# Kernel tuning notes

Hardware: AMD Instinct MI355X
Metric: run time of the kernel (lower is better)

## Reference

```python
import jax, jax.numpy as jnp
import numpy as np

E, H, I, K, T = 8, 1024, 2816, 2, 2048


def setup_inputs() -> dict:
    key = jax.random.key(0)
    k1, k2, k3, k4, k5, k6 = jax.random.split(key, 6)
    hidden_states = jax.random.normal(k1, (T, H), dtype=jnp.float32)
    top_k_indices = jax.random.randint(k2, (T, K), 0, E, dtype=jnp.int32)
    raw = jax.random.uniform(k3, (T, K), dtype=jnp.float32) + 0.1
    top_k_values = raw / jnp.sum(raw, axis=-1, keepdims=True)  # router softmax-like weights
    scale = 1.0 / np.sqrt(H)
    w_gate = jax.random.normal(k4, (E, H, I), dtype=jnp.float32) * scale
    w_up = jax.random.normal(k5, (E, H, I), dtype=jnp.float32) * scale
    w_down = jax.random.normal(k6, (E, I, H), dtype=jnp.float32) * (1.0 / np.sqrt(I))
    return {
        "hidden_states": hidden_states,
        "top_k_indices": top_k_indices,
        "top_k_values": top_k_values,
        "w_gate": w_gate,
        "w_up": w_up,
        "w_down": w_down,
    }


def reference(hidden_states, top_k_indices, top_k_values, w_gate, w_up, w_down):
    # Each expert: SwiGLU FFN  down( silu(x @ gate) * (x @ up) )
    # Run every expert on every token (dense reference for grouped-GEMM dispatch),
    # then combine with the per-token top-k routing weights.
    def expert(wg, wu, wd):
        g = jnp.matmul(hidden_states, wg)          # [T, I]
        u = jnp.matmul(hidden_states, wu)          # [T, I]
        return jnp.matmul(jax.nn.silu(g) * u, wd)  # [T, H]

    y = jax.vmap(expert)(w_gate, w_up, w_down)     # [E, T, H]

    t = hidden_states.shape[0]
    # comb[t, e] = sum over k of top_k_values[t, k] where top_k_indices[t, k] == e
    comb = jnp.zeros((t, w_gate.shape[0]), dtype=hidden_states.dtype)
    comb = comb.at[jnp.arange(t)[:, None], top_k_indices].add(top_k_values)
    out = jnp.einsum('te,eth->th', comb, y)        # weighted combine -> [T, H]
    return out
```

## Files before the change

kernel.cpp:

```cpp
#include <hip/hip_runtime.h>
#include <stdint.h>

#define T_TOK 2048
#define KTOP  2
#define NEXP  8
#define HDIM  1024
#define IDIM  2816

#define NPAIR 4096

#define BM        128
#define MAX_TILES 40
#define NPP       (NPAIR + BM)
#define BN2       128
#define BK2       32
#define BN3       64
#define BK3       64
#define GUB       (MAX_TILES * (IDIM / BN2))
#define CVB       ((IDIM / 64) * (HDIM / 64) * NEXP)

#define R1BM   256
#define R1T    24
#define R1NPP  (NPAIR + R1BM)
#define R1BN2  128
#define R1BK2  32
#define R1BKp2 40
#define R1BN3  64
#define R1BK3  64
#define R1BKp3 72

typedef __attribute__((ext_vector_type(8))) short short8;
typedef __attribute__((ext_vector_type(4))) float floatx4;

__device__ __forceinline__ unsigned short f2bf(float f) {
  unsigned int u = __float_as_uint(f);
  u += 0x7fffu + ((u >> 16) & 1u);
  return (unsigned short)(u >> 16);
}

__device__ __forceinline__ unsigned int pkbf(float a, float b) {
  unsigned int r;
  asm volatile("v_cvt_pk_bf16_f32 %0, %1, %2" : "=v"(r) : "v"(a), "v"(b));
  return r;
}

__device__ __forceinline__ void glds16(const unsigned short* g, unsigned short* l) {
  __builtin_amdgcn_global_load_lds(
      (const __attribute__((address_space(1))) unsigned int*)g,
      (__attribute__((address_space(3))) unsigned int*)l, 16, 0, 0);
}

__device__ __forceinline__ int xcd_tile(int bx0) {
  return (bx0 & 7) * (MAX_TILES / 8) + (bx0 >> 3);
}

__global__ void setup_kernel(const int* __restrict__ idx,
                             const float* __restrict__ vals,
                             int* __restrict__ hdr,
                             int* __restrict__ stok,
                             float* __restrict__ sw, int bm) {
  __shared__ int cnt[NEXP];
  __shared__ int off[NEXP];
  int tid = threadIdx.x;
  if (tid < NEXP) cnt[tid] = 0;
  __syncthreads();
  for (int p = tid; p < NPAIR; p += blockDim.x) atomicAdd(&cnt[idx[p]], 1);
  __syncthreads();
  if (tid == 0) {
    int s = 0, nt = 0;
    for (int e = 0; e < NEXP; ++e) {
      off[e] = s;
      int n = cnt[e];
      for (int t0 = 0; t0 < n; t0 += bm) {
        hdr[nt] = e;
        hdr[64 + nt] = s + t0;
        hdr[128 + nt] = s + n;
        nt++;
      }
      s += n;
    }
    for (; nt < 64; ++nt) hdr[nt] = -1;
  }
  __syncthreads();
  for (int p = tid; p < NPAIR; p += blockDim.x) {
    int e = idx[p];
    int pos = atomicAdd(&off[e], 1);
    stok[pos] = p / KTOP;
    sw[pos] = vals[p];
  }
}

__global__ void gather_kernel(const float* __restrict__ hidden,
                              const int* __restrict__ stok,
                              unsigned short* __restrict__ Xs) {
  int p = blockIdx.x;
  int t = stok[p];
  const float4* src = reinterpret_cast<const float4*>(hidden + (size_t)t * HDIM);
  float4 v = src[threadIdx.x];
  uint2 q;
  q.x = pkbf(v.x, v.y);
  q.y = pkbf(v.z, v.w);
  *reinterpret_cast<uint2*>(Xs + (size_t)p * HDIM + threadIdx.x * 4) = q;
}

__global__ __launch_bounds__(256) void convert_kernel(
    const float* __restrict__ wg, const float* __restrict__ wu,
    const float* __restrict__ wd, unsigned short* __restrict__ wgT,
    unsigned short* __restrict__ wuT, unsigned short* __restrict__ wdT,
    int zoff) {
  __shared__ float ls[64][65];
  int z = blockIdx.z + zoff;
  int e = blockIdx.y;
  int M = (z == 2) ? IDIM : HDIM;
  int N = (z == 2) ? HDIM : IDIM;
  const float* src = (z == 0 ? wg : z == 1 ? wu : wd) + (size_t)e * M * N;
  unsigned short* dst = (z == 0 ? wgT : z == 1 ? wuT : wdT) + (size_t)e * M * N;
  int ntx = N >> 6;
  int n0 = (blockIdx.x % ntx) << 6;
  int m0 = (blockIdx.x / ntx) << 6;
  int t = threadIdx.x;
  int rr = t >> 4, cc = (t & 15) * 4;
#pragma unroll
  for (int i = 0; i < 4; ++i) {
    int r = rr + i * 16;
    float4 v = *reinterpret_cast<const float4*>(src + (size_t)(m0 + r) * N + n0 + cc);
    ls[r][cc] = v.x; ls[r][cc + 1] = v.y; ls[r][cc + 2] = v.z; ls[r][cc + 3] = v.w;
  }
  __syncthreads();
  int mc = (t & 7) * 8, nn = t >> 3;
#pragma unroll
  for (int i = 0; i < 2; ++i) {
    int n = nn + i * 32;
    uint4 q;
    q.x = pkbf(ls[mc][n],     ls[mc + 1][n]);
    q.y = pkbf(ls[mc + 2][n], ls[mc + 3][n]);
    q.z = pkbf(ls[mc + 4][n], ls[mc + 5][n]);
    q.w = pkbf(ls[mc + 6][n], ls[mc + 7][n]);
    *reinterpret_cast<uint4*>(dst + (size_t)(n0 + n) * M + m0 + mc) = q;
  }
}

__global__ __launch_bounds__(256, 2) void gateup_kernel(
    const unsigned short* __restrict__ Xs, const unsigned short* __restrict__ wgT,
    const unsigned short* __restrict__ wuT, const int* __restrict__ hdr,
    const float* __restrict__ sw_g, unsigned short* __restrict__ Act,
    const float* __restrict__ wd, unsigned short* __restrict__ wdT) {
  __shared__ __align__(16) char smem[25088];

  if (blockIdx.x >= GUB) {
    int cb = blockIdx.x - GUB;
    int e = cb / ((IDIM / 64) * (HDIM / 64));
    int bq = cb % ((IDIM / 64) * (HDIM / 64));
    const int ntx = HDIM >> 6;
    int n0 = (bq % ntx) << 6;
    int m0 = (bq / ntx) << 6;
    const float* src = wd + (size_t)e * IDIM * HDIM;
    unsigned short* dst = wdT + (size_t)e * IDIM * HDIM;
    float (*ls)[65] = reinterpret_cast<float(*)[65]>(smem);
    int t = threadIdx.x;
    int rr = t >> 4, cc = (t & 15) * 4;
#pragma unroll
    for (int i = 0; i < 4; ++i) {
      int r = rr + i * 16;
      float4 v = *reinterpret_cast<const float4*>(src + (size_t)(m0 + r) * HDIM + n0 + cc);
      ls[r][cc] = v.x; ls[r][cc + 1] = v.y; ls[r][cc + 2] = v.z; ls[r][cc + 3] = v.w;
    }
    __syncthreads();
    int mc = (t & 7) * 8, nn = t >> 3;
#pragma unroll
    for (int i = 0; i < 2; ++i) {
      int n = nn + i * 32;
      uint4 q;
      q.x = pkbf(ls[mc][n],     ls[mc + 1][n]);
      q.y = pkbf(ls[mc + 2][n], ls[mc + 3][n]);
      q.z = pkbf(ls[mc + 4][n], ls[mc + 5][n]);
      q.w = pkbf(ls[mc + 6][n], ls[mc + 7][n]);
      *reinterpret_cast<uint4*>(dst + (size_t)(n0 + n) * IDIM + m0 + mc) = q;
    }
    return;
  }

  int mx = blockIdx.x % MAX_TILES;
  int ny = blockIdx.x / MAX_TILES;
  int bx = xcd_tile(mx);
  int e = hdr[bx];
  if (e < 0) return;
  int row0 = hdr[64 + bx];
  int rowlim = hdr[128 + bx] - row0;
  int n0 = ny * BN2;

  unsigned short* As = reinterpret_cast<unsigned short*>(smem);
  unsigned short* Bg = reinterpret_cast<unsigned short*>(smem + 8192);
  unsigned short* Bu = reinterpret_cast<unsigned short*>(smem + 16384);
  float* sw = reinterpret_cast<float*>(smem + 24576);

  int tid = threadIdx.x, lane = tid & 63, wave = tid >> 6;
  if (tid < BM) sw[tid] = sw_g[row0 + tid];

  const unsigned short* wgb = wgT + (size_t)e * IDIM * HDIM;
  const unsigned short* wub = wuT + (size_t)e * IDIM * HDIM;

  floatx4 accg[4][4], accu[4][4];
  floatx4 zz = {0.f, 0.f, 0.f, 0.f};
#pragma unroll
  for (int a = 0; a < 4; ++a)
#pragma unroll
    for (int b = 0; b < 4; ++b) { accg[a][b] = zz; accu[a][b] = zz; }

  int wm = (wave >> 1) * 64, wn = (wave & 1) * 64;
  int lr = lane >> 2;
  int lk = (((lane & 3) ^ ((lr >> 1) & 3)) * 8);
  int fr = lane & 15;
  int fq = (((lane >> 4) ^ ((fr >> 1) & 3)) * 8);

  for (int kb = 0; kb < HDIM; kb += BK2) {
#pragma unroll
    for (int it = 0; it < 2; ++it) {
      int c = wave * 2 + it;
      glds16(Xs  + (size_t)(row0 + c * 16 + lr) * HDIM + kb + lk, &As[c * 512]);
      glds16(wgb + (size_t)(n0  + c * 16 + lr) * HDIM + kb + lk, &Bg[c * 512]);
      glds16(wub + (size_t)(n0  + c * 16 + lr) * HDIM + kb + lk, &Bu[c * 512]);
    }
    __syncthreads();

    short8 af[4], bg8[4], bu8[4];
#pragma unroll
    for (int x = 0; x < 4; ++x) {
      af[x]  = *reinterpret_cast<const short8*>(&As[(wm + x * 16 + fr) * BK2 + fq]);
      bg8[x] = *reinterpret_cast<const short8*>(&Bg[(wn + x * 16 + fr) * BK2 + fq]);
      bu8[x] = *reinterpret_cast<const short8*>(&Bu[(wn + x * 16 + fr) * BK2 + fq]);
    }
#pragma unroll
    for (int tm = 0; tm < 4; ++tm)
#pragma unroll
      for (int tn = 0; tn < 4; ++tn) {
        accg[tm][tn] = __builtin_amdgcn_mfma_f32_16x16x32_bf16(af[tm], bg8[tn], accg[tm][tn], 0, 0, 0);
        accu[tm][tn] = __builtin_amdgcn_mfma_f32_16x16x32_bf16(af[tm], bu8[tn], accu[tm][tn], 0, 0, 0);
      }
    __syncthreads();
  }

#pragma unroll
  for (int tm = 0; tm < 4; ++tm)
#pragma unroll
    for (int tn = 0; tn < 4; ++tn)
#pragma unroll
      for (int r = 0; r < 4; ++r) {
        int rl = wm + tm * 16 + (lane >> 4) * 4 + r;
        if (rl < rowlim) {
          int col = n0 + wn + tn * 16 + fr;
          float g = accg[tm][tn][r];
          float u = accu[tm][tn][r];
          float s = g / (1.f + __expf(-g));
          Act[(size_t)(row0 + rl) * IDIM + col] = f2bf(s * u * sw[rl]);
        }
      }
}

__global__ __launch_bounds__(256, 3) void down_kernel(
    const unsigned short* __restrict__ Act, const unsigned short* __restrict__ wdT,
    const int* __restrict__ hdr, const int* __restrict__ stok,
    float* __restrict__ out) {
  int bx = xcd_tile(blockIdx.x);
  int e = hdr[bx];
  if (e < 0) return;
  int row0 = hdr[64 + bx];
  int rowlim = hdr[128 + bx] - row0;
  int n0 = blockIdx.y * BN3;

  __shared__ __align__(16) unsigned short As[BM * BK3];
  __shared__ __align__(16) unsigned short Bd[BN3 * BK3];
  __shared__ int stk[BM];

  int tid = threadIdx.x, lane = tid & 63, wave = tid >> 6;
  if (tid < BM) stk[tid] = stok[row0 + tid];

  const unsigned short* wdb = wdT + (size_t)e * HDIM * IDIM;

  floatx4 acc[4][2];
  floatx4 zz = {0.f, 0.f, 0.f, 0.f};
#pragma unroll
  for (int a = 0; a < 4; ++a) { acc[a][0] = zz; acc[a][1] = zz; }

  int wm = (wave >> 1) * 64, wn = (wave & 1) * 32;
  int lr8 = lane >> 3;
  int lk8 = (((lane & 7) ^ lr8) * 8);
  int fr = lane & 15;
  int fk = fr & 7;

  for (int kb = 0; kb < IDIM; kb += BK3) {
#pragma unroll
    for (int it = 0; it < 4; ++it) {
      int c = wave * 4 + it;
      glds16(Act + (size_t)(row0 + c * 8 + lr8) * IDIM + kb + lk8, &As[c * 512]);
    }
#pragma unroll
    for (int it = 0; it < 2; ++it) {
      int c = wave * 2 + it;
      glds16(wdb + (size_t)(n0 + c * 8 + lr8) * IDIM + kb + lk8, &Bd[c * 512]);
    }
    __syncthreads();

#pragma unroll
    for (int ks = 0; ks < BK3; ks += 32) {
      int q8 = (ks >> 3) + (lane >> 4);
      int fo = ((q8 ^ fk) * 8);
      short8 af[4], bd8[2];
#pragma unroll
      for (int x = 0; x < 4; ++x)
        af[x] = *reinterpret_cast<const short8*>(&As[(wm + x * 16 + fr) * BK3 + fo]);
#pragma unroll
      for (int x = 0; x < 2; ++x)
        bd8[x] = *reinterpret_cast<const short8*>(&Bd[(wn + x * 16 + fr) * BK3 + fo]);
#pragma unroll
      for (int tm = 0; tm < 4; ++tm)
#pragma unroll
        for (int tn = 0; tn < 2; ++tn)
          acc[tm][tn] = __builtin_amdgcn_mfma_f32_16x16x32_bf16(af[tm], bd8[tn], acc[tm][tn], 0, 0, 0);
    }
    __syncthreads();
  }

#pragma unroll
  for (int tm = 0; tm < 4; ++tm)
#pragma unroll
    for (int tn = 0; tn < 2; ++tn)
#pragma unroll
      for (int r = 0; r < 4; ++r) {
        int rl = wm + tm * 16 + (lane >> 4) * 4 + r;
        if (rl < rowlim) {
          int col = n0 + wn + tn * 16 + fr;
          unsafeAtomicAdd(&out[(size_t)stk[rl] * HDIM + col], acc[tm][tn][r]);
        }
      }
}

__global__ __launch_bounds__(512, 2) void gateup_fb(
    const unsigned short* __restrict__ Xs, const float* __restrict__ wg,
    const float* __restrict__ wu, const int* __restrict__ hdr,
    const float* __restrict__ sw_g, unsigned short* __restrict__ Act) {
  int by = blockIdx.y;
  int e = hdr[by];
  if (e < 0) return;
  int row0 = hdr[64 + by];
  int row_end = hdr[128 + by];
  int n0 = blockIdx.x * R1BN2;

  __shared__ __align__(16) unsigned short As[R1BM * R1BKp2];
  __shared__ __align__(16) unsigned short Bg[R1BN2 * R1BKp2];
  __shared__ __align__(16) unsigned short Bu[R1BN2 * R1BKp2];
  __shared__ float sw[R1BM];

  int tid = threadIdx.x, lane = tid & 63, wave = tid >> 6;
  if (tid < R1BM) sw[tid] = sw_g[row0 + tid];

  const float* wgb = wg + (size_t)e * HDIM * IDIM;
  const float* wub = wu + (size_t)e * HDIM * IDIM;

  floatx4 accg[4][4], accu[4][4];
  floatx4 zz = {0.f, 0.f, 0.f, 0.f};
#pragma unroll
  for (int a = 0; a < 4; ++a)
#pragma unroll
    for (int b = 0; b < 4; ++b) { accg[a][b] = zz; accu[a][b] = zz; }

  int wm = (wave >> 1) * 64, wn = (wave & 1) * 64;

  for (int kb = 0; kb < HDIM; kb += R1BK2) {
    __syncthreads();
#pragma unroll
    for (int it = 0; it < 2; ++it) {
      int cc = wave * 2 + it;
      int m = cc * 16 + (lane >> 2);
      int k = (lane & 3) * 8;
      uint4 v = *reinterpret_cast<const uint4*>(Xs + (size_t)(row0 + m) * HDIM + kb + k);
      *reinterpret_cast<uint4*>(&As[m * R1BKp2 + k]) = v;
    }
#pragma unroll
    for (int it = 0; it < 2; ++it) {
      int cc = wave * 2 + it;
      const float* wb = (cc & 8) ? wub : wgb;
      unsigned short* Bs = (cc & 8) ? Bu : Bg;
      int r = cc & 7;
      int kblk = r >> 1, nh = r & 1;
      int n = nh * 64 + lane;
      int k = kblk * 8;
      const float* src = wb + (size_t)(kb + k) * IDIM + n0 + n;
      uint4 q;
      q.x = f2bf(src[0])                | ((unsigned)f2bf(src[(size_t)IDIM])     << 16);
      q.y = f2bf(src[2 * (size_t)IDIM]) | ((unsigned)f2bf(src[3 * (size_t)IDIM]) << 16);
      q.z = f2bf(src[4 * (size_t)IDIM]) | ((unsigned)f2bf(src[5 * (size_t)IDIM]) << 16);
      q.w = f2bf(src[6 * (size_t)IDIM]) | ((unsigned)f2bf(src[7 * (size_t)IDIM]) << 16);
      *reinterpret_cast<uint4*>(&Bs[n * R1BKp2 + k]) = q;
    }
    __syncthreads();

    int krd = (lane >> 4) * 8;
    short8 af[4], bgf[4], buf_[4];
#pragma unroll
    for (int tm = 0; tm < 4; ++tm)
      af[tm] = *reinterpret_cast<const short8*>(&As[(wm + tm * 16 + (lane & 15)) * R1BKp2 + krd]);
#pragma unroll
    for (int tn = 0; tn < 4; ++tn) {
      bgf[tn]  = *reinterpret_cast<const short8*>(&Bg[(wn + tn * 16 + (lane & 15)) * R1BKp2 + krd]);
      buf_[tn] = *reinterpret_cast<const short8*>(&Bu[(wn + tn * 16 + (lane & 15)) * R1BKp2 + krd]);
    }
#pragma unroll
    for (int tm = 0; tm < 4; ++tm)
#pragma unroll
      for (int tn = 0; tn < 4; ++tn) {
        accg[tm][tn] = __builtin_amdgcn_mfma_f32_16x16x32_bf16(af[tm], bgf[tn], accg[tm][tn], 0, 0, 0);
        accu[tm][tn] = __builtin_amdgcn_mfma_f32_16x16x32_bf16(af[tm], buf_[tn], accu[tm][tn], 0, 0, 0);
      }
  }

  int rowlim = row_end - row0;
#pragma unroll
  for (int tm = 0; tm < 4; ++tm)
#pragma unroll
    for (int tn = 0; tn < 4; ++tn)
#pragma unroll
      for (int r = 0; r < 4; ++r) {
        int rl = wm + tm * 16 + (lane >> 4) * 4 + r;
        if (rl < rowlim) {
          int col = n0 + wn + tn * 16 + (lane & 15);
          float g = accg[tm][tn][r];
          float u = accu[tm][tn][r];
          float s = g / (1.f + __expf(-g));
          Act[(size_t)(row0 + rl) * IDIM + col] = f2bf(s * u * sw[rl]);
        }
      }
}

__global__ __launch_bounds__(512, 2) void down_fb(
    const unsigned short* __restrict__ Act, const float* __restrict__ wd,
    const int* __restrict__ hdr, const int* __restrict__ stok,
    float* __restrict__ out) {
  int by = blockIdx.y;
  int e = hdr[by];
  if (e < 0) return;
  int row0 = hdr[64 + by];
  int row_end = hdr[128 + by];
  int n0 = blockIdx.x * R1BN3;

  __shared__ __align__(16) unsigned short As[R1BM * R1BKp3];
  __shared__ __align__(16) unsigned short Bd[R1BN3 * R1BKp3];
  __shared__ int stk[R1BM];

  int tid = threadIdx.x, lane = tid & 63, wave = tid >> 6;
  if (tid < R1BM) stk[tid] = stok[row0 + tid];

  const float* wdb = wd + (size_t)e * IDIM * HDIM;

  floatx4 acc[4][2];
  floatx4 zz = {0.f, 0.f, 0.f, 0.f};
#pragma unroll
  for (int a = 0; a < 4; ++a) { acc[a][0] = zz; acc[a][1] = zz; }

  int wm = (wave >> 1) * 64, wn = (wave & 1) * 32;

  for (int kb = 0; kb < IDIM; kb += R1BK3) {
    __syncthreads();
#pragma unroll
    for (int it = 0; it < 4; ++it) {
      int cc = wave * 4 + it;
      int m = cc * 8 + (lane >> 3);
      int k = (lane & 7) * 8;
      uint4 v = *reinterpret_cast<const uint4*>(Act + (size_t)(row0 + m) * IDIM + kb + k);
      *reinterpret_cast<uint4*>(&As[m * R1BKp3 + k]) = v;
    }
    {
      int n = lane;
      int k = wave * 8;
      const float* src = wdb + (size_t)(kb + k) * HDIM + n0 + n;
      uint4 q;
      q.x = f2bf(src[0])        | ((unsigned)f2bf(src[HDIM])     << 16);
      q.y = f2bf(src[2 * HDIM]) | ((unsigned)f2bf(src[3 * HDIM]) << 16);
      q.z = f2bf(src[4 * HDIM]) | ((unsigned)f2bf(src[5 * HDIM]) << 16);
      q.w = f2bf(src[6 * HDIM]) | ((unsigned)f2bf(src[7 * HDIM]) << 16);
      *reinterpret_cast<uint4*>(&Bd[n * R1BKp3 + k]) = q;
    }
    __syncthreads();

#pragma unroll
    for (int ks = 0; ks < R1BK3; ks += 32) {
      int krd = ks + (lane >> 4) * 8;
      short8 af[4], bdf[2];
#pragma unroll
      for (int tm = 0; tm < 4; ++tm)
        af[tm] = *reinterpret_cast<const short8*>(&As[(wm + tm * 16 + (lane & 15)) * R1BKp3 + krd]);
#pragma unroll
      for (int tn = 0; tn < 2; ++tn)
        bdf[tn] = *reinterpret_cast<const short8*>(&Bd[(wn + tn * 16 + (lane & 15)) * R1BKp3 + krd]);
#pragma unroll
      for (int tm = 0; tm < 4; ++tm)
#pragma unroll
        for (int tn = 0; tn < 2; ++tn)
          acc[tm][tn] = __builtin_amdgcn_mfma_f32_16x16x32_bf16(af[tm], bdf[tn], acc[tm][tn], 0, 0, 0);
    }
  }

  int rowlim = row_end - row0;
#pragma unroll
  for (int tm = 0; tm < 4; ++tm)
#pragma unroll
    for (int tn = 0; tn < 2; ++tn)
#pragma unroll
      for (int r = 0; r < 4; ++r) {
        int rl = wm + tm * 16 + (lane >> 4) * 4 + r;
        if (rl < rowlim) {
          int col = n0 + wn + tn * 16 + (lane & 15);
          unsafeAtomicAdd(&out[(size_t)stk[rl] * HDIM + col], acc[tm][tn][r]);
        }
      }
}

extern "C" void kernel_launch(void* const* d_in, const int* in_sizes, int n_in,
                              void* d_out, int out_size, void* d_ws, size_t ws_size,
                              hipStream_t stream) {
  const float* hidden = (const float*)d_in[0];
  const int* idx = (const int*)d_in[1];
  const float* vals = (const float*)d_in[2];
  const float* wg = (const float*)d_in[3];
  const float* wu = (const float*)d_in[4];
  const float* wd = (const float*)d_in[5];
  float* out = (float*)d_out;
  char* ws = (char*)d_ws;

  hipMemsetAsync(d_out, 0, (size_t)out_size * sizeof(float), stream);

  const size_t OFF_STOK = 4096;
  const size_t OFF_SW   = OFF_STOK + (size_t)NPP * 4;
  const size_t OFF_XS   = 65536;
  const size_t OFF_ACT  = OFF_XS + (size_t)NPP * HDIM * 2;
  const size_t OFF_WG   = OFF_ACT + (size_t)NPP * IDIM * 2;
  const size_t WSZ      = (size_t)NEXP * HDIM * IDIM * 2;
  const size_t OFF_WU   = OFF_WG + WSZ;
  const size_t OFF_WD   = OFF_WU + WSZ;
  const size_t NEED     = OFF_WD;
  const size_t NEED2    = OFF_WD + WSZ;

  if (ws_size >= NEED) {
    int* hdr = (int*)ws;
    int* stok = (int*)(ws + OFF_STOK);
    float* sw = (float*)(ws + OFF_SW);
    unsigned short* Xs  = (unsigned short*)(ws + OFF_XS);
    unsigned short* Act = (unsigned short*)(ws + OFF_ACT);
    unsigned short* wgT = (unsigned short*)(ws + OFF_WG);
    unsigned short* wuT = (unsigned short*)(ws + OFF_WU);
    bool sep = (ws_size >= NEED2);
    unsigned short* wdT = sep ? (unsigned short*)(ws + OFF_WD) : wgT;

    setup_kernel<<<1, 1024, 0, stream>>>(idx, vals, hdr, stok, sw, BM);
    convert_kernel<<<dim3(704, NEXP, 2), 256, 0, stream>>>(wg, wu, wd, wgT, wuT, wdT, 0);
    gather_kernel<<<NPAIR, 256, 0, stream>>>(hidden, stok, Xs);
    if (sep) {
      gateup_kernel<<<GUB + CVB, 256, 0, stream>>>(Xs, wgT, wuT, hdr, sw, Act, wd, wdT);
    } else {
      gateup_kernel<<<GUB, 256, 0, stream>>>(Xs, wgT, wuT, hdr, sw, Act, wd, wdT);
      convert_kernel<<<dim3(704, NEXP, 1), 256, 0, stream>>>(wg, wu, wd, wgT, wuT, wdT, 2);
    }
    down_kernel<<<dim3(MAX_TILES, HDIM / BN3), 256, 0, stream>>>(Act, wdT, hdr, stok, out);
  } else {
    int* hdr = (int*)ws;
    int* stok = (int*)(ws + 4096);
    float* sw = (float*)(ws + 4096 + (size_t)R1NPP * 4);
    unsigned short* Xs  = (unsigned short*)(ws + 65536);
    unsigned short* Act = (unsigned short*)(ws + 65536 + (size_t)R1NPP * HDIM * 2);

    setup_kernel<<<1, 1024, 0, stream>>>(idx, vals, hdr, stok, sw, R1BM);
    gather_kernel<<<NPAIR, 256, 0, stream>>>(hidden, stok, Xs);
    gateup_fb<<<dim3(IDIM / R1BN2, R1T), 512, 0, stream>>>(Xs, wg, wu, hdr, sw, Act);
    down_fb<<<dim3(HDIM / R1BN3, R1T), 512, 0, stream>>>(Act, wd, hdr, stok, out);
  }
}
```

Baseline: 420.3 us.

## Split weight conversion and gate/up GEMM into halves, overlap; split-K down GEMM

The initial weight conversion now only transposes the first half of the gate/up columns. The gate/up GEMM is split into two launches over column halves. The first launch also converts the remaining gate/up halves, and the second converts w_down, so conversion overlaps with matmul work. The down GEMM uses a 128-wide N tile with split-K over two halves of I, accumulating through the existing atomics, and its occupancy hint is raised. This adds an extra launch and more atomic traffic, and ordering across launches is what keeps the converted weights ready in time.

Result: no change. 420.2 us (-0.0%).

```diff
diff --git a/kernel.cpp b/kernel.cpp
--- a/kernel.cpp
+++ b/kernel.cpp
@@ -14,10 +14,11 @@
 #define NPP       (NPAIR + BM)
 #define BN2       128
 #define BK2       32
-#define BN3       64
+#define BN3       128
 #define BK3       64
-#define GUB       (MAX_TILES * (IDIM / BN2))
-#define CVB       ((IDIM / 64) * (HDIM / 64) * NEXP)
+#define NYH       11
+#define GUBH      (MAX_TILES * NYH)
+#define CVT       5632
 
 #define R1BM   256
 #define R1T    24
@@ -107,7 +108,7 @@
     const float* __restrict__ wg, const float* __restrict__ wu,
     const float* __restrict__ wd, unsigned short* __restrict__ wgT,
     unsigned short* __restrict__ wuT, unsigned short* __restrict__ wdT,
-    int zoff) {
+    int zoff, int ioff, int intx) {
   __shared__ float ls[64][65];
   int z = blockIdx.z + zoff;
   int e = blockIdx.y;
@@ -115,9 +116,8 @@
   int N = (z == 2) ? HDIM : IDIM;
   const float* src = (z == 0 ? wg : z == 1 ? wu : wd) + (size_t)e * M * N;
   unsigned short* dst = (z == 0 ? wgT : z == 1 ? wuT : wdT) + (size_t)e * M * N;
-  int ntx = N >> 6;
-  int n0 = (blockIdx.x % ntx) << 6;
-  int m0 = (blockIdx.x / ntx) << 6;
+  int n0 = ((blockIdx.x % intx) + ioff) << 6;
+  int m0 = (blockIdx.x / intx) << 6;
   int t = threadIdx.x;
   int rr = t >> 4, cc = (t & 15) * 4;
 #pragma unroll
@@ -144,25 +144,43 @@
     const unsigned short* __restrict__ Xs, const unsigned short* __restrict__ wgT,
     const unsigned short* __restrict__ wuT, const int* __restrict__ hdr,
     const float* __restrict__ sw_g, unsigned short* __restrict__ Act,
-    const float* __restrict__ wd, unsigned short* __restrict__ wdT) {
+    const float* __restrict__ wg, const float* __restrict__ wu,
+    const float* __restrict__ wd, unsigned short* __restrict__ wgTw,
+    unsigned short* __restrict__ wuTw, unsigned short* __restrict__ wdTw,
+    int mode) {
   __shared__ __align__(16) char smem[25088];
 
-  if (blockIdx.x >= GUB) {
-    int cb = blockIdx.x - GUB;
-    int e = cb / ((IDIM / 64) * (HDIM / 64));
-    int bq = cb % ((IDIM / 64) * (HDIM / 64));
-    const int ntx = HDIM >> 6;
-    int n0 = (bq % ntx) << 6;
-    int m0 = (bq / ntx) << 6;
-    const float* src = wd + (size_t)e * IDIM * HDIM;
-    unsigned short* dst = wdT + (size_t)e * IDIM * HDIM;
+  if (blockIdx.x >= GUBH) {
+    int cb = blockIdx.x - GUBH;
+    const float* src;
+    unsigned short* dst;
+    int n0, m0, rdN, wrM;
+    if (mode == 0) {
+      int z = cb / 2816;
+      int rem = cb - z * 2816;
+      int e = rem / 352;
+      int bq = rem % 352;
+      n0 = ((bq % 22) + 22) << 6;
+      m0 = (bq / 22) << 6;
+      rdN = IDIM; wrM = HDIM;
+      src = (z ? wu : wg) + (size_t)e * HDIM * IDIM;
+      dst = (z ? wuTw : wgTw) + (size_t)e * IDIM * HDIM;
+    } else {
+      int e = cb / 704;
+      int bq = cb % 704;
+      n0 = (bq % 16) << 6;
+      m0 = (bq / 16) << 6;
+      rdN = HDIM; wrM = IDIM;
+      src = wd + (size_t)e * IDIM * HDIM;
+      dst = wdTw + (size_t)e * IDIM * HDIM;
+    }
     float (*ls)[65] = reinterpret_cast<float(*)[65]>(smem);
     int t = threadIdx.x;
     int rr = t >> 4, cc = (t & 15) * 4;
 #pragma unroll
     for (int i = 0; i < 4; ++i) {
       int r = rr + i * 16;
-      float4 v = *reinterpret_cast<const float4*>(src + (size_t)(m0 + r) * HDIM + n0 + cc);
+      float4 v = *reinterpret_cast<const float4*>(src + (size_t)(m0 + r) * rdN + n0 + cc);
       ls[r][cc] = v.x; ls[r][cc + 1] = v.y; ls[r][cc + 2] = v.z; ls[r][cc + 3] = v.w;
     }
     __syncthreads();
@@ -175,13 +193,13 @@
       q.y = pkbf(ls[mc + 2][n], ls[mc + 3][n]);
       q.z = pkbf(ls[mc + 4][n], ls[mc + 5][n]);
       q.w = pkbf(ls[mc + 6][n], ls[mc + 7][n]);
-      *reinterpret_cast<uint4*>(dst + (size_t)(n0 + n) * IDIM + m0 + mc) = q;
+      *reinterpret_cast<uint4*>(dst + (size_t)(n0 + n) * wrM + m0 + mc) = q;
     }
     return;
   }
 
   int mx = blockIdx.x % MAX_TILES;
-  int ny = blockIdx.x / MAX_TILES;
+  int ny = blockIdx.x / MAX_TILES + mode * NYH;
   int bx = xcd_tile(mx);
   int e = hdr[bx];
   if (e < 0) return;
@@ -257,7 +275,7 @@
       }
 }
 
-__global__ __launch_bounds__(256, 3) void down_kernel(
+__global__ __launch_bounds__(256, 4) void down_kernel(
     const unsigned short* __restrict__ Act, const unsigned short* __restrict__ wdT,
     const int* __restrict__ hdr, const int* __restrict__ stok,
     float* __restrict__ out) {
@@ -267,6 +285,8 @@
   int row0 = hdr[64 + bx];
   int rowlim = hdr[128 + bx] - row0;
   int n0 = blockIdx.y * BN3;
+  int kb0 = blockIdx.z * (IDIM / 2);
+  int kend = kb0 + (IDIM / 2);
 
   __shared__ __align__(16) unsigned short As[BM * BK3];
   __shared__ __align__(16) unsigned short Bd[BN3 * BK3];
@@ -277,27 +297,25 @@
 
   const unsigned short* wdb = wdT + (size_t)e * HDIM * IDIM;
 
-  floatx4 acc[4][2];
+  floatx4 acc[4][4];
   floatx4 zz = {0.f, 0.f, 0.f, 0.f};
 #pragma unroll
-  for (int a = 0; a < 4; ++a) { acc[a][0] = zz; acc[a][1] = zz; }
-
-  int wm = (wave >> 1) * 64, wn = (wave & 1) * 32;
+  for (int a = 0; a < 4; ++a)
+#pragma unroll
+    for (int b = 0; b < 4; ++b) acc[a][b] = zz;
+
+  int wm = (wave >> 1) * 64, wn = (wave & 1) * 64;
   int lr8 = lane >> 3;
   int lk8 = (((lane & 7) ^ lr8) * 8);
   int fr = lane & 15;
   int fk = fr & 7;
 
-  for (int kb = 0; kb < IDIM; kb += BK3) {
+  for (int kb = kb0; kb < kend; kb += BK3) {
 #pragma unroll
     for (int it = 0; it < 4; ++it) {
       int c = wave * 4 + it;
       glds16(Act + (size_t)(row0 + c * 8 + lr8) * IDIM + kb + lk8, &As[c * 512]);
-    }
-#pragma unroll
-    for (int it = 0; it < 2; ++it) {
-      int c = wave * 2 + it;
-      glds16(wdb + (size_t)(n0 + c * 8 + lr8) * IDIM + kb + lk8, &Bd[c * 512]);
+      glds16(wdb + (size_t)(n0  + c * 8 + lr8) * IDIM + kb + lk8, &Bd[c * 512]);
     }
     __syncthreads();
 
@@ -305,17 +323,16 @@
     for (int ks = 0; ks < BK3; ks += 32) {
       int q8 = (ks >> 3) + (lane >> 4);
       int fo = ((q8 ^ fk) * 8);
-      short8 af[4], bd8[2];
-#pragma unroll
-      for (int x = 0; x < 4; ++x)
-        af[x] = *reinterpret_cast<const short8*>(&As[(wm + x * 16 + fr) * BK3 + fo]);
-#pragma unroll
-      for (int x = 0; x < 2; ++x)
+      short8 af[4], bd8[4];
+#pragma unroll
+      for (int x = 0; x < 4; ++x) {
+        af[x]  = *reinterpret_cast<const short8*>(&As[(wm + x * 16 + fr) * BK3 + fo]);
         bd8[x] = *reinterpret_cast<const short8*>(&Bd[(wn + x * 16 + fr) * BK3 + fo]);
+      }
 #pragma unroll
       for (int tm = 0; tm < 4; ++tm)
 #pragma unroll
-        for (int tn = 0; tn < 2; ++tn)
+        for (int tn = 0; tn < 4; ++tn)
           acc[tm][tn] = __builtin_amdgcn_mfma_f32_16x16x32_bf16(af[tm], bd8[tn], acc[tm][tn], 0, 0, 0);
     }
     __syncthreads();
@@ -324,7 +341,7 @@
 #pragma unroll
   for (int tm = 0; tm < 4; ++tm)
 #pragma unroll
-    for (int tn = 0; tn < 2; ++tn)
+    for (int tn = 0; tn < 4; ++tn)
 #pragma unroll
       for (int r = 0; r < 4; ++r) {
         int rl = wm + tm * 16 + (lane >> 4) * 4 + r;
@@ -552,15 +569,22 @@
     unsigned short* wdT = sep ? (unsigned short*)(ws + OFF_WD) : wgT;
 
     setup_kernel<<<1, 1024, 0, stream>>>(idx, vals, hdr, stok, sw, BM);
-    convert_kernel<<<dim3(704, NEXP, 2), 256, 0, stream>>>(wg, wu, wd, wgT, wuT, wdT, 0);
+    convert_kernel<<<dim3(352, NEXP, 2), 256, 0, stream>>>(
+        wg, wu, wd, wgT, wuT, wdT, 0, 0, 22);
     gather_kernel<<<NPAIR, 256, 0, stream>>>(hidden, stok, Xs);
+    gateup_kernel<<<GUBH + CVT, 256, 0, stream>>>(
+        Xs, wgT, wuT, hdr, sw, Act, wg, wu, wd, wgT, wuT, wdT, 0);
     if (sep) {
-      gateup_kernel<<<GUB + CVB, 256, 0, stream>>>(Xs, wgT, wuT, hdr, sw, Act, wd, wdT);
+      gateup_kernel<<<GUBH + CVT, 256, 0, stream>>>(
+          Xs, wgT, wuT, hdr, sw, Act, wg, wu, wd, wgT, wuT, wdT, 1);
     } else {
-      gateup_kernel<<<GUB, 256, 0, stream>>>(Xs, wgT, wuT, hdr, sw, Act, wd, wdT);
-      convert_kernel<<<dim3(704, NEXP, 1), 256, 0, stream>>>(wg, wu, wd, wgT, wuT, wdT, 2);
-    }
-    down_kernel<<<dim3(MAX_TILES, HDIM / BN3), 256, 0, stream>>>(Act, wdT, hdr, stok, out);
+      gateup_kernel<<<GUBH, 256, 0, stream>>>(
+          Xs, wgT, wuT, hdr, sw, Act, wg, wu, wd, wgT, wuT, wdT, 1);
+      convert_kernel<<<dim3(704, NEXP, 1), 256, 0, stream>>>(
+          wg, wu, wd, wgT, wuT, wdT, 2, 0, 16);
+    }
+    down_kernel<<<dim3(MAX_TILES, HDIM / BN3, 2), 256, 0, stream>>>(
+        Act, wdT, hdr, stok, out);
   } else {
     int* hdr = (int*)ws;
     int* stok = (int*)(ws + 4096);
```
